# Kernel optimization log

Hardware: AMD Instinct MI355X
Metric: run time of the kernel (lower is better)

The kernel has to match this reference:

```python
import jax, jax.numpy as jnp
import numpy as np
from jax import lax

B, C, O, H, W = 4, 96, 96, 128, 128
K = 3      # kernel size everywhere
D = 2      # dilation of dconv
KK = K * K


def conv2d(x, w, b, pad, dil=1):
    # x: [B,C,H,W], w: [O,C,K,K]
    y = lax.conv_general_dilated(
        x, w, window_strides=(1, 1), padding=[(pad, pad), (pad, pad)],
        rhs_dilation=(dil, dil), dimension_numbers=('NCHW', 'OIHW', 'NCHW'))
    return y + b[None, :, None, None]


def bilinear_sample(img, py, px):
    # img: [B,C,H,W]; py,px: [B,KK,H,W] float sample coords (zero outside)
    y0 = jnp.floor(py)
    x0 = jnp.floor(px)
    wy = py - y0
    wx = px - x0
    flat = img.reshape(B, 1, C, H * W)  # broadcast over KK

    def gather(yi, xi):
        valid = (yi >= 0) & (yi < H) & (xi >= 0) & (xi < W)
        yc = jnp.clip(yi, 0, H - 1).astype(jnp.int32)
        xc = jnp.clip(xi, 0, W - 1).astype(jnp.int32)
        idx = (yc * W + xc).reshape(B, KK, 1, H * W)
        g = jnp.take_along_axis(flat, idx, axis=3)  # [B,KK,C,H*W]
        g = g.reshape(B, KK, C, H, W)
        return g * valid.reshape(B, KK, 1, H, W)

    v00 = gather(y0, x0)
    v01 = gather(y0, x0 + 1)
    v10 = gather(y0 + 1, x0)
    v11 = gather(y0 + 1, x0 + 1)
    wy = wy[:, :, None]
    wx = wx[:, :, None]
    return ((1 - wy) * ((1 - wx) * v00 + wx * v01)
            + wy * ((1 - wx) * v10 + wx * v11))


def setup_inputs() -> dict:
    key = jax.random.key(0)
    ks = jax.random.split(key, 7)
    x = jax.random.normal(ks[0], (B, C, H, W), jnp.float32)
    s = 1.0 / np.sqrt(C * K * K)  # torch default conv init bound
    u = lambda k, shape: jax.random.uniform(k, shape, jnp.float32, -s, s)
    return dict(
        x=x,
        dconv_w=u(ks[1], (O, C, K, K)), dconv_b=u(ks[2], (O,)),
        off_w=u(ks[3], (2 * KK, C, K, K)), off_b=u(ks[4], (2 * KK,)),
        def_w=u(ks[5], (O, C, K, K)), def_b=u(ks[6], (O,)),
    )


def reference(x, dconv_w, dconv_b, off_w, off_b, def_w, def_b):
    # dilated conv + relu + residual (self.conv is unused in the original forward)
    x1 = conv2d(x, dconv_w, dconv_b, pad=D, dil=D)
    x3 = x + jax.nn.relu(x1)

    # offset prediction: [B, 2*KK, H, W] -> (dy, dx) per kernel tap
    offset = conv2d(x3, off_w, off_b, pad=1)
    off = offset.reshape(B, KK, 2, H, W)
    dy, dx = off[:, :, 0], off[:, :, 1]

    # base sampling grid: output pixel + kernel tap - padding
    ki, kj = jnp.meshgrid(jnp.arange(K), jnp.arange(K), indexing='ij')
    ky = (ki.reshape(-1) - (K - 1) // 2).astype(jnp.float32)  # [KK]
    kx = (kj.reshape(-1) - (K - 1) // 2).astype(jnp.float32)
    ygrid = jnp.arange(H, dtype=jnp.float32)[:, None]
    xgrid = jnp.arange(W, dtype=jnp.float32)[None, :]
    py = ygrid[None, None] + ky[None, :, None, None] + dy  # [B,KK,H,W]
    px = xgrid[None, None] + kx[None, :, None, None] + dx

    sampled = bilinear_sample(x3, py, px)  # [B,KK,C,H,W]
    out = jnp.einsum('bkchw,ock->bohw', sampled, def_w.reshape(O, C, KK))
    return out + def_b[None, :, None, None]
```

## Files before the change

### kernel.cpp

```cpp
#include <hip/hip_runtime.h>
#include <hip/hip_bf16.h>

#define BD 4
#define CD 96
#define OD 96
#define HD 128
#define WD 128
#define HWD (HD*WD)

typedef __attribute__((ext_vector_type(8))) short bfrag;
typedef __attribute__((ext_vector_type(4))) float ffrag;

__device__ __forceinline__ short f2bs(float f) {
    __hip_bfloat16 h = __float2bfloat16(f);
    return *reinterpret_cast<short*>(&h);
}

__device__ __forceinline__ int swizzle256(int gid) {
    return ((gid & 7) << 5) | (gid >> 3);
}

__global__ __launch_bounds__(256) void k_transpose(const float* __restrict__ x,
                                                   short* __restrict__ xb16) {
    __shared__ short tile[64 * 104];
    int pix0 = blockIdx.x * 64;
    int b = pix0 / HWD; int hw0 = pix0 % HWD;
    int tid = threadIdx.x;

    for (int e = tid; e < 96*16; e += 256) {
        int c = e >> 4, g = e & 15;
        float4 v = *(const float4*)(x + ((size_t)(b*96 + c))*HWD + hw0 + 4*g);
        tile[(4*g+0)*104 + c] = f2bs(v.x);
        tile[(4*g+1)*104 + c] = f2bs(v.y);
        tile[(4*g+2)*104 + c] = f2bs(v.z);
        tile[(4*g+3)*104 + c] = f2bs(v.w);
    }
    __syncthreads();
    for (int e = tid; e < 64*12; e += 256) {
        int px = e / 12, c8 = e % 12;
        bfrag v = *(const bfrag*)(tile + px*104 + c8*8);
        *(bfrag*)(xb16 + ((size_t)(pix0 + px))*96 + c8*8) = v;
    }
}

__global__ void k_repack(const float* __restrict__ dconv_w,
                         const float* __restrict__ off_w,
                         const float* __restrict__ def_w,
                         short* __restrict__ wB1,
                         short* __restrict__ wB2,
                         short* __restrict__ wB) {
    int t = blockIdx.x * blockDim.x + threadIdx.x;
    if (t < 27648) {
        int j = t & 7; int l = (t >> 3) & 63; int tile = t >> 9;
        int s = tile >> 1, nt = tile & 1;
        int k = 32*s + (l >> 4)*8 + j;
        int o = 16*nt + (l & 15);
        int c = k % 96, tap = k / 96;
        wB2[t] = (o < 18) ? f2bs(off_w[(o*96 + c)*9 + tap]) : (short)0;
    }
    if (t < 82944) {
        int j = t & 7; int l = (t >> 3) & 63; int tile = t >> 9;
        int s = tile / 6, nt = tile % 6;
        int k = 32*s + (l >> 4)*8 + j;
        int o = 16*nt + (l & 15);
        int c = k % 96, tap = k / 96;
        wB1[t] = f2bs(dconv_w[(o*96 + c)*9 + tap]);
        wB[t]  = f2bs(def_w [(o*96 + c)*9 + tap]);
    }
}

#define SLICE_SHORTS 9216

__global__ __launch_bounds__(512, 2) void k_conv1(const float* __restrict__ x,
                                                  const short* __restrict__ xb16,
                                                  const short* __restrict__ wB,
                                                  const float* __restrict__ bias,
                                                  short* __restrict__ x3b) {
    __shared__ short wbuf[2][SLICE_SHORTS];

    int pix0 = swizzle256(blockIdx.x) * 256;
    int b = pix0 / HWD; int hw0 = pix0 % HWD;
    int h0 = hw0 / WD;
    int tid = threadIdx.x;
    int l = tid & 63, wv = tid >> 6;
    int q = l >> 4, mr = l & 15;
    const char* xbc = (const char*)(xb16 + ((size_t)b * HWD) * 96);
    const bfrag az = {0,0,0,0,0,0,0,0};

    int lpb[2], yb[2], wbx[2];
    #pragma unroll
    for (int mt = 0; mt < 2; mt++) {
        lpb[mt] = 32*wv + 16*mt;
        yb[mt]  = h0 + (lpb[mt] >> 7);
        wbx[mt] = (lpb[mt] & 127) + mr;
    }

    {
        bfrag s0, s1, s2;
        int c0 = tid, c1 = tid + 512, c2 = tid + 1024;
        s0 = *(const bfrag*)(wB + c0*8);
        s1 = *(const bfrag*)(wB + c1*8);
        if (c2 < 1152) s2 = *(const bfrag*)(wB + c2*8);
        *(bfrag*)&wbuf[0][c0*8] = s0;
        *(bfrag*)&wbuf[0][c1*8] = s1;
        if (c2 < 1152) *(bfrag*)&wbuf[0][c2*8] = s2;
    }
    __syncthreads();

    ffrag acc[2][6];
    #pragma unroll
    for (int mt = 0; mt < 2; mt++)
        #pragma unroll
        for (int nt = 0; nt < 6; nt++) acc[mt][nt] = ffrag{0.f,0.f,0.f,0.f};

    int cur = 0;
    #pragma unroll 1
    for (int tap = 0; tap < 9; tap++) {
        bfrag s0, s1, s2;
        if (tap < 8) {
            const short* src = wB + (size_t)(tap+1)*SLICE_SHORTS;
            int c2 = tid + 1024;
            s0 = *(const bfrag*)(src + tid*8);
            s1 = *(const bfrag*)(src + (tid+512)*8);
            if (c2 < 1152) s2 = *(const bfrag*)(src + c2*8);
        }

        int ty = (tap/3)*2 - 2, tx = (tap%3)*2 - 2;
        #pragma unroll
        for (int mt = 0; mt < 2; mt++) {
            int y = yb[mt] + ty;
            bool vy = (unsigned)y < HD;
            int yc = min(max(y, 0), HD-1);
            int xx = wbx[mt] + tx;
            int xxc = min(max(xx, 0), WD-1);
            bool v = vy && ((unsigned)xx < WD);
            unsigned aoff = (unsigned)(((yc*WD + xxc)*96 + q*8) * 2);
            #pragma unroll
            for (int sc = 0; sc < 3; sc++) {
                bfrag a = *(const bfrag*)(xbc + aoff + sc*64);
                if (!v) a = az;
                const short* wp = &wbuf[cur][(sc*6)*512 + l*8];
                #pragma unroll
                for (int nt = 0; nt < 6; nt++) {
                    bfrag bb = *(const bfrag*)(wp + nt*512);
                    acc[mt][nt] = __builtin_amdgcn_mfma_f32_16x16x32_bf16(a, bb, acc[mt][nt], 0, 0, 0);
                }
            }
        }

        if (tap < 8) {
            int c2 = tid + 1024;
            *(bfrag*)&wbuf[cur^1][tid*8]       = s0;
            *(bfrag*)&wbuf[cur^1][(tid+512)*8] = s1;
            if (c2 < 1152) *(bfrag*)&wbuf[cur^1][c2*8] = s2;
        }
        __syncthreads();
        cur ^= 1;
    }

    #pragma unroll
    for (int mt = 0; mt < 2; mt++) {
        int hwb = hw0 + lpb[mt] + q*4;
        #pragma unroll
        for (int nt = 0; nt < 6; nt++) {
            int o = 16*nt + mr;
            float bo = bias[o];
            float4 xr = *(const float4*)(x + ((size_t)(b*96 + o))*HWD + hwb);
            short* op = x3b + ((size_t)(b*HWD + hwb))*96 + o;
            op[0]   = f2bs(xr.x + fmaxf(acc[mt][nt][0] + bo, 0.f));
            op[96]  = f2bs(xr.y + fmaxf(acc[mt][nt][1] + bo, 0.f));
            op[192] = f2bs(xr.z + fmaxf(acc[mt][nt][2] + bo, 0.f));
            op[288] = f2bs(xr.w + fmaxf(acc[mt][nt][3] + bo, 0.f));
        }
    }
}

__global__ __launch_bounds__(512, 2) void k_deform(const short* __restrict__ x3b,
                                                   const short* __restrict__ wB2,
                                                   const float* __restrict__ off_b,
                                                   const short* __restrict__ wB,
                                                   const float* __restrict__ def_b,
                                                   float* __restrict__ out) {
    __shared__ short wbuf[2][SLICE_SHORTS];
    __shared__ float offsb[256][20];

    int pix0 = swizzle256(blockIdx.x) * 256;
    int b = pix0 / HWD; int hw0 = pix0 % HWD;
    int h0 = hw0 / WD;
    int tid = threadIdx.x;
    int l = tid & 63, wv = tid >> 6;
    int q = l >> 4, mr = l & 15;
    const char* xbc = (const char*)(x3b + ((size_t)b * HWD) * 96);
    const bfrag az = {0,0,0,0,0,0,0,0};

    int lpb[2], yb[2], wbx[2];
    #pragma unroll
    for (int mt = 0; mt < 2; mt++) {
        lpb[mt] = 32*wv + 16*mt;
        yb[mt]  = h0 + (lpb[mt] >> 7);
        wbx[mt] = (lpb[mt] & 127) + mr;
    }

    {
        bfrag s0, s1, s2;
        int c2 = tid + 1024;
        s0 = *(const bfrag*)(wB + tid*8);
        s1 = *(const bfrag*)(wB + (tid+512)*8);
        if (c2 < 1152) s2 = *(const bfrag*)(wB + c2*8);
        *(bfrag*)&wbuf[0][tid*8]       = s0;
        *(bfrag*)&wbuf[0][(tid+512)*8] = s1;
        if (c2 < 1152) *(bfrag*)&wbuf[0][c2*8] = s2;
    }
    __syncthreads();

    ffrag oa[2][2];
    #pragma unroll
    for (int mt = 0; mt < 2; mt++)
        #pragma unroll
        for (int nt = 0; nt < 2; nt++) oa[mt][nt] = ffrag{0.f,0.f,0.f,0.f};

    #pragma unroll 1
    for (int tap = 0; tap < 9; tap++) {
        int ty = tap/3 - 1, tx = tap%3 - 1;
        #pragma unroll
        for (int mt = 0; mt < 2; mt++) {
            int y = yb[mt] + ty;
            bool vy = (unsigned)y < HD;
            int yc = min(max(y, 0), HD-1);
            int xx = wbx[mt] + tx;
            int xxc = min(max(xx, 0), WD-1);
            bool v = vy && ((unsigned)xx < WD);
            unsigned aoff = (unsigned)(((yc*WD + xxc)*96 + q*8) * 2);
            #pragma unroll
            for (int sc = 0; sc < 3; sc++) {
                const short* wb = wB2 + ((size_t)((tap*3+sc)*2)*64 + l)*8;
                bfrag b0 = *(const bfrag*)(wb);
                bfrag b1 = *(const bfrag*)(wb + 512);
                bfrag a = *(const bfrag*)(xbc + aoff + sc*64);
                if (!v) a = az;
                oa[mt][0] = __builtin_amdgcn_mfma_f32_16x16x32_bf16(a, b0, oa[mt][0], 0, 0, 0);
                oa[mt][1] = __builtin_amdgcn_mfma_f32_16x16x32_bf16(a, b1, oa[mt][1], 0, 0, 0);
            }
        }
    }
    #pragma unroll
    for (int mt = 0; mt < 2; mt++) {
        int row = lpb[mt] + q*4;
        float bo0 = off_b[mr];
        #pragma unroll
        for (int r = 0; r < 4; r++) offsb[row + r][mr] = oa[mt][0][r] + bo0;
        if (mr < 2) {
            float bo1 = off_b[16 + mr];
            #pragma unroll
            for (int r = 0; r < 4; r++) offsb[row + r][16 + mr] = oa[mt][1][r] + bo1;
        }
    }

    ffrag acc[2][6];
    #pragma unroll
    for (int mt = 0; mt < 2; mt++)
        #pragma unroll
        for (int nt = 0; nt < 6; nt++) acc[mt][nt] = ffrag{0.f,0.f,0.f,0.f};

    int cur = 0;
    #pragma unroll 1
    for (int tap = 0; tap < 9; tap++) {
        bfrag s0, s1, s2;
        if (tap < 8) {
            const short* src = wB + (size_t)(tap+1)*SLICE_SHORTS;
            int c2 = tid + 1024;
            s0 = *(const bfrag*)(src + tid*8);
            s1 = *(const bfrag*)(src + (tid+512)*8);
            if (c2 < 1152) s2 = *(const bfrag*)(src + c2*8);
        }

        unsigned po[2][4];
        float fb[2][4];
        #pragma unroll
        for (int mt = 0; mt < 2; mt++) {
            int lp = lpb[mt] + mr;
            float dy = offsb[lp][2*tap];
            float dx = offsb[lp][2*tap + 1];
            float py  = (float)(yb[mt]  + tap/3 - 1) + dy;
            float pxf = (float)(wbx[mt] + tap%3 - 1) + dx;
            float y0f = floorf(py), x0f = floorf(pxf);
            float wy = py - y0f, wx = pxf - x0f;
            int y0 = (int)y0f, x0 = (int)x0f;
            int y1 = y0 + 1, x1 = x0 + 1;
            bool vy0 = (unsigned)y0 < HD, vy1 = (unsigned)y1 < HD;
            bool vx0 = (unsigned)x0 < WD, vx1 = (unsigned)x1 < WD;
            fb[mt][0] = (vy0 && vx0) ? (1.f-wy)*(1.f-wx) : 0.f;
            fb[mt][1] = (vy0 && vx1) ? (1.f-wy)*wx       : 0.f;
            fb[mt][2] = (vy1 && vx0) ? wy*(1.f-wx)       : 0.f;
            fb[mt][3] = (vy1 && vx1) ? wy*wx             : 0.f;
            int yc0 = min(max(y0,0),HD-1), yc1 = min(max(y1,0),HD-1);
            int xc0 = min(max(x0,0),WD-1), xc1 = min(max(x1,0),WD-1);
            po[mt][0] = (unsigned)(((yc0*WD + xc0)*96 + q*8)*2);
            po[mt][1] = (unsigned)(((yc0*WD + xc1)*96 + q*8)*2);
            po[mt][2] = (unsigned)(((yc1*WD + xc0)*96 + q*8)*2);
            po[mt][3] = (unsigned)(((yc1*WD + xc1)*96 + q*8)*2);
        }
        #pragma unroll
        for (int sc = 0; sc < 3; sc++) {
            const short* wp = &wbuf[cur][(sc*6)*512 + l*8];
            bfrag bbf[6];
            #pragma unroll
            for (int nt = 0; nt < 6; nt++) bbf[nt] = *(const bfrag*)(wp + nt*512);
            #pragma unroll
            for (int mt = 0; mt < 2; mt++) {
                bfrag c00 = *(const bfrag*)(xbc + po[mt][0] + sc*64);
                bfrag c01 = *(const bfrag*)(xbc + po[mt][1] + sc*64);
                bfrag c10 = *(const bfrag*)(xbc + po[mt][2] + sc*64);
                bfrag c11 = *(const bfrag*)(xbc + po[mt][3] + sc*64);
                const int* i00 = (const int*)&c00;
                const int* i01 = (const int*)&c01;
                const int* i10 = (const int*)&c10;
                const int* i11 = (const int*)&c11;
                float f00 = fb[mt][0], f01 = fb[mt][1];
                float f10 = fb[mt][2], f11 = fb[mt][3];
                int ap[4];
                #pragma unroll
                for (int d = 0; d < 4; d++) {
                    float a0 = __int_as_float(((unsigned)i00[d]) << 16);
                    float b0f = __int_as_float(((unsigned)i01[d]) << 16);
                    float c0f = __int_as_float(((unsigned)i10[d]) << 16);
                    float d0 = __int_as_float(((unsigned)i11[d]) << 16);
                    float a1 = __int_as_float(i00[d] & 0xffff0000);
                    float b1f = __int_as_float(i01[d] & 0xffff0000);
                    float c1f = __int_as_float(i10[d] & 0xffff0000);
                    float d1 = __int_as_float(i11[d] & 0xffff0000);
                    float rlo = f00*a0 + f01*b0f + f10*c0f + f11*d0;
                    float rhi = f00*a1 + f01*b1f + f10*c1f + f11*d1;
                    ap[d] = (int)((unsigned short)f2bs(rlo)) |
                            ((int)((unsigned short)f2bs(rhi)) << 16);
                }
                bfrag a = *(const bfrag*)ap;
                #pragma unroll
                for (int nt = 0; nt < 6; nt++)
                    acc[mt][nt] = __builtin_amdgcn_mfma_f32_16x16x32_bf16(a, bbf[nt], acc[mt][nt], 0, 0, 0);
            }
        }

        if (tap < 8) {
            int c2 = tid + 1024;
            *(bfrag*)&wbuf[cur^1][tid*8]       = s0;
            *(bfrag*)&wbuf[cur^1][(tid+512)*8] = s1;
            if (c2 < 1152) *(bfrag*)&wbuf[cur^1][c2*8] = s2;
        }
        __syncthreads();
        cur ^= 1;
    }

    #pragma unroll
    for (int mt = 0; mt < 2; mt++) {
        int hwb = hw0 + lpb[mt] + q*4;
        #pragma unroll
        for (int nt = 0; nt < 6; nt++) {
            int o = 16*nt + mr;
            float bo = def_b[o];
            float4 v;
            v.x = acc[mt][nt][0] + bo; v.y = acc[mt][nt][1] + bo;
            v.z = acc[mt][nt][2] + bo; v.w = acc[mt][nt][3] + bo;
            *(float4*)(out + ((size_t)(b*96 + o))*HWD + hwb) = v;
        }
    }
}

extern "C" void kernel_launch(void* const* d_in, const int* in_sizes, int n_in,
                              void* d_out, int out_size, void* d_ws, size_t ws_size,
                              hipStream_t stream) {
    const float* x       = (const float*)d_in[0];
    const float* dconv_w = (const float*)d_in[1];
    const float* dconv_b = (const float*)d_in[2];
    const float* off_w   = (const float*)d_in[3];
    const float* off_b   = (const float*)d_in[4];
    const float* def_w   = (const float*)d_in[5];
    const float* def_b   = (const float*)d_in[6];
    float* out = (float*)d_out;

    char* ws = (char*)d_ws;
    short* xb16 = (short*)(ws);
    short* x3b  = (short*)(ws + 12582912);
    short* wB1  = (short*)(ws + 25165824);
    short* wB2  = (short*)(ws + 25331712);
    short* wB   = (short*)(ws + 25387008);

    k_repack<<<324, 256, 0, stream>>>(dconv_w, off_w, def_w, wB1, wB2, wB);
    k_transpose<<<(BD*HWD)/64, 256, 0, stream>>>(x, xb16);
    k_conv1<<<(BD*HWD)/256, 512, 0, stream>>>(x, xb16, wB1, dconv_b, x3b);
    k_deform<<<(BD*HWD)/256, 512, 0, stream>>>(x3b, wB2, off_b, wB, def_b, out);
}
```

Baseline: 162.3 us.

## Stage x3 epilogue via LDS, LDS-buffer offset weights, prefetch next-tap gathers

The dconv epilogue now stages bf16 x3 results in an LDS tile and writes full 16-byte channel vectors per pixel, replacing scattered 2-byte global stores. In the deform kernel, offset-conv weights are double-buffered in shared memory instead of being read from global inside the MFMA loop. The first channel chunk of the next tap's bilinear gathers is prefetched during the current tap to hide gather latency. The cost is more shared memory, extra barriers in the offset loop, and higher register pressure from the prefetched fragments, which may reduce occupancy under launch bounds of 512 threads and 2 blocks.

```diff
diff --git a/kernel.cpp b/kernel.cpp
--- a/kernel.cpp
+++ b/kernel.cpp
@@ -14,6 +14,31 @@
 __device__ __forceinline__ short f2bs(float f) {
     __hip_bfloat16 h = __float2bfloat16(f);
     return *reinterpret_cast<short*>(&h);
+}
+
+__device__ __forceinline__ bfrag interp4(bfrag c00, bfrag c01, bfrag c10, bfrag c11,
+                                         float f00, float f01, float f10, float f11) {
+    const int* i00 = (const int*)&c00;
+    const int* i01 = (const int*)&c01;
+    const int* i10 = (const int*)&c10;
+    const int* i11 = (const int*)&c11;
+    int ap[4];
+    #pragma unroll
+    for (int d = 0; d < 4; d++) {
+        float a0 = __int_as_float(((unsigned)i00[d]) << 16);
+        float b0 = __int_as_float(((unsigned)i01[d]) << 16);
+        float c0 = __int_as_float(((unsigned)i10[d]) << 16);
+        float d0 = __int_as_float(((unsigned)i11[d]) << 16);
+        float a1 = __int_as_float(i00[d] & 0xffff0000);
+        float b1 = __int_as_float(i01[d] & 0xffff0000);
+        float c1 = __int_as_float(i10[d] & 0xffff0000);
+        float d1 = __int_as_float(i11[d] & 0xffff0000);
+        float rlo = f00*a0 + f01*b0 + f10*c0 + f11*d0;
+        float rhi = f00*a1 + f01*b1 + f10*c1 + f11*d1;
+        ap[d] = (int)((unsigned short)f2bs(rlo)) |
+                ((int)((unsigned short)f2bs(rhi)) << 16);
+    }
+    return *(const bfrag*)ap;
 }
 
 __device__ __forceinline__ int swizzle256(int gid) {
@@ -97,12 +122,12 @@
 
     {
         bfrag s0, s1, s2;
-        int c0 = tid, c1 = tid + 512, c2 = tid + 1024;
-        s0 = *(const bfrag*)(wB + c0*8);
-        s1 = *(const bfrag*)(wB + c1*8);
+        int c2 = tid + 1024;
+        s0 = *(const bfrag*)(wB + tid*8);
+        s1 = *(const bfrag*)(wB + (tid+512)*8);
         if (c2 < 1152) s2 = *(const bfrag*)(wB + c2*8);
-        *(bfrag*)&wbuf[0][c0*8] = s0;
-        *(bfrag*)&wbuf[0][c1*8] = s1;
+        *(bfrag*)&wbuf[0][tid*8]       = s0;
+        *(bfrag*)&wbuf[0][(tid+512)*8] = s1;
         if (c2 < 1152) *(bfrag*)&wbuf[0][c2*8] = s2;
     }
     __syncthreads();
@@ -158,20 +183,33 @@
         cur ^= 1;
     }
 
-    #pragma unroll
-    for (int mt = 0; mt < 2; mt++) {
-        int hwb = hw0 + lpb[mt] + q*4;
-        #pragma unroll
-        for (int nt = 0; nt < 6; nt++) {
-            int o = 16*nt + mr;
-            float bo = bias[o];
-            float4 xr = *(const float4*)(x + ((size_t)(b*96 + o))*HWD + hwb);
-            short* op = x3b + ((size_t)(b*HWD + hwb))*96 + o;
-            op[0]   = f2bs(xr.x + fmaxf(acc[mt][nt][0] + bo, 0.f));
-            op[96]  = f2bs(xr.y + fmaxf(acc[mt][nt][1] + bo, 0.f));
-            op[192] = f2bs(xr.z + fmaxf(acc[mt][nt][2] + bo, 0.f));
-            op[288] = f2bs(xr.w + fmaxf(acc[mt][nt][3] + bo, 0.f));
-        }
+    short (*etile)[104] = (short(*)[104])&wbuf[0][0];
+    #pragma unroll 1
+    for (int ph = 0; ph < 2; ph++) {
+        #pragma unroll
+        for (int mt = 0; mt < 2; mt++) {
+            if ((lpb[mt] >> 7) == ph) {
+                int lrow = (lpb[mt] & 127) + q*4;
+                int hwb = hw0 + 128*ph + lrow;
+                #pragma unroll
+                for (int nt = 0; nt < 6; nt++) {
+                    int o = 16*nt + mr;
+                    float bo = bias[o];
+                    float4 xr = *(const float4*)(x + ((size_t)(b*96 + o))*HWD + hwb);
+                    etile[lrow+0][o] = f2bs(xr.x + fmaxf(acc[mt][nt][0] + bo, 0.f));
+                    etile[lrow+1][o] = f2bs(xr.y + fmaxf(acc[mt][nt][1] + bo, 0.f));
+                    etile[lrow+2][o] = f2bs(xr.z + fmaxf(acc[mt][nt][2] + bo, 0.f));
+                    etile[lrow+3][o] = f2bs(xr.w + fmaxf(acc[mt][nt][3] + bo, 0.f));
+                }
+            }
+        }
+        __syncthreads();
+        for (int e = tid; e < 128*12; e += 512) {
+            int px = e / 12, c8 = e % 12;
+            bfrag v = *(const bfrag*)&etile[px][c8*8];
+            *(bfrag*)(x3b + ((size_t)(b*HWD + hw0 + 128*ph + px))*96 + c8*8) = v;
+        }
+        __syncthreads();
     }
 }
 
@@ -181,8 +219,10 @@
                                                    const short* __restrict__ wB,
                                                    const float* __restrict__ def_b,
                                                    float* __restrict__ out) {
-    __shared__ short wbuf[2][SLICE_SHORTS];
-    __shared__ float offsb[256][20];
+    __shared__ __align__(16) char smem[36864 + 20480];
+    short (*wbuf)[SLICE_SHORTS] = (short(*)[SLICE_SHORTS])smem;
+    short* cb = (short*)(smem + 36864);
+    float (*offsb)[20] = (float(*)[20])(smem + 36864);
 
     int pix0 = swizzle256(blockIdx.x) * 256;
     int b = pix0 / HWD; int hw0 = pix0 % HWD;
@@ -210,6 +250,10 @@
         *(bfrag*)&wbuf[0][tid*8]       = s0;
         *(bfrag*)&wbuf[0][(tid+512)*8] = s1;
         if (c2 < 1152) *(bfrag*)&wbuf[0][c2*8] = s2;
+        if (tid < 384) {
+            bfrag sc2 = *(const bfrag*)(wB2 + tid*8);
+            *(bfrag*)&cb[tid*8] = sc2;
+        }
     }
     __syncthreads();
 
@@ -219,8 +263,13 @@
         #pragma unroll
         for (int nt = 0; nt < 2; nt++) oa[mt][nt] = ffrag{0.f,0.f,0.f,0.f};
 
+    int c2cur = 0;
     #pragma unroll 1
     for (int tap = 0; tap < 9; tap++) {
+        bfrag sn;
+        bool act = (tid < 384) && (tap < 8);
+        if (act) sn = *(const bfrag*)(wB2 + (size_t)(tap+1)*3072 + tid*8);
+
         int ty = tap/3 - 1, tx = tap%3 - 1;
         #pragma unroll
         for (int mt = 0; mt < 2; mt++) {
@@ -233,7 +282,7 @@
             unsigned aoff = (unsigned)(((yc*WD + xxc)*96 + q*8) * 2);
             #pragma unroll
             for (int sc = 0; sc < 3; sc++) {
-                const short* wb = wB2 + ((size_t)((tap*3+sc)*2)*64 + l)*8;
+                const short* wb = cb + c2cur*3072 + (sc*2)*512 + l*8;
                 bfrag b0 = *(const bfrag*)(wb);
                 bfrag b1 = *(const bfrag*)(wb + 512);
                 bfrag a = *(const bfrag*)(xbc + aoff + sc*64);
@@ -242,7 +291,12 @@
                 oa[mt][1] = __builtin_amdgcn_mfma_f32_16x16x32_bf16(a, b1, oa[mt][1], 0, 0, 0);
             }
         }
-    }
+
+        if (act) *(bfrag*)&cb[(c2cur^1)*3072 + tid*8] = sn;
+        __syncthreads();
+        c2cur ^= 1;
+    }
+
     #pragma unroll
     for (int mt = 0; mt < 2; mt++) {
         int row = lpb[mt] + q*4;
@@ -262,20 +316,7 @@
         #pragma unroll
         for (int nt = 0; nt < 6; nt++) acc[mt][nt] = ffrag{0.f,0.f,0.f,0.f};
 
-    int cur = 0;
-    #pragma unroll 1
-    for (int tap = 0; tap < 9; tap++) {
-        bfrag s0, s1, s2;
-        if (tap < 8) {
-            const short* src = wB + (size_t)(tap+1)*SLICE_SHORTS;
-            int c2 = tid + 1024;
-            s0 = *(const bfrag*)(src + tid*8);
-            s1 = *(const bfrag*)(src + (tid+512)*8);
-            if (c2 < 1152) s2 = *(const bfrag*)(src + c2*8);
-        }
-
-        unsigned po[2][4];
-        float fb[2][4];
+    auto prep = [&](int tap, unsigned (&po)[2][4], float (&fbv)[2][4]) {
         #pragma unroll
         for (int mt = 0; mt < 2; mt++) {
             int lp = lpb[mt] + mr;
@@ -289,10 +330,10 @@
             int y1 = y0 + 1, x1 = x0 + 1;
             bool vy0 = (unsigned)y0 < HD, vy1 = (unsigned)y1 < HD;
             bool vx0 = (unsigned)x0 < WD, vx1 = (unsigned)x1 < WD;
-            fb[mt][0] = (vy0 && vx0) ? (1.f-wy)*(1.f-wx) : 0.f;
-            fb[mt][1] = (vy0 && vx1) ? (1.f-wy)*wx       : 0.f;
-            fb[mt][2] = (vy1 && vx0) ? wy*(1.f-wx)       : 0.f;
-            fb[mt][3] = (vy1 && vx1) ? wy*wx             : 0.f;
+            fbv[mt][0] = (vy0 && vx0) ? (1.f-wy)*(1.f-wx) : 0.f;
+            fbv[mt][1] = (vy0 && vx1) ? (1.f-wy)*wx       : 0.f;
+            fbv[mt][2] = (vy1 && vx0) ? wy*(1.f-wx)       : 0.f;
+            fbv[mt][3] = (vy1 && vx1) ? wy*wx             : 0.f;
             int yc0 = min(max(y0,0),HD-1), yc1 = min(max(y1,0),HD-1);
             int xc0 = min(max(x0,0),WD-1), xc1 = min(max(x1,0),WD-1);
             po[mt][0] = (unsigned)(((yc0*WD + xc0)*96 + q*8)*2);
@@ -300,8 +341,53 @@
             po[mt][2] = (unsigned)(((yc1*WD + xc0)*96 + q*8)*2);
             po[mt][3] = (unsigned)(((yc1*WD + xc1)*96 + q*8)*2);
         }
-        #pragma unroll
-        for (int sc = 0; sc < 3; sc++) {
+    };
+
+    unsigned po[2][4]; float fbv[2][4];
+    prep(0, po, fbv);
+    bfrag cpre[8];
+    #pragma unroll
+    for (int mt = 0; mt < 2; mt++)
+        #pragma unroll
+        for (int k = 0; k < 4; k++)
+            cpre[mt*4+k] = *(const bfrag*)(xbc + po[mt][k]);
+
+    int cur = 0;
+    #pragma unroll 1
+    for (int tap = 0; tap < 9; tap++) {
+        bfrag s0, s1, s2;
+        if (tap < 8) {
+            const short* src = wB + (size_t)(tap+1)*SLICE_SHORTS;
+            int c2 = tid + 1024;
+            s0 = *(const bfrag*)(src + tid*8);
+            s1 = *(const bfrag*)(src + (tid+512)*8);
+            if (c2 < 1152) s2 = *(const bfrag*)(src + c2*8);
+        }
+        unsigned pon[2][4]; float fbn[2][4]; bfrag cnx[8];
+        if (tap < 8) {
+            prep(tap+1, pon, fbn);
+            #pragma unroll
+            for (int mt = 0; mt < 2; mt++)
+                #pragma unroll
+                for (int k = 0; k < 4; k++)
+                    cnx[mt*4+k] = *(const bfrag*)(xbc + pon[mt][k]);
+        }
+        {
+            const short* wp = &wbuf[cur][0*512 + l*8];
+            bfrag bbf[6];
+            #pragma unroll
+            for (int nt = 0; nt < 6; nt++) bbf[nt] = *(const bfrag*)(wp + nt*512);
+            #pragma unroll
+            for (int mt = 0; mt < 2; mt++) {
+                bfrag a = interp4(cpre[mt*4+0], cpre[mt*4+1], cpre[mt*4+2], cpre[mt*4+3],
+                                  fbv[mt][0], fbv[mt][1], fbv[mt][2], fbv[mt][3]);
+                #pragma unroll
+                for (int nt = 0; nt < 6; nt++)
+                    acc[mt][nt] = __builtin_amdgcn_mfma_f32_16x16x32_bf16(a, bbf[nt], acc[mt][nt], 0, 0, 0);
+            }
+        }
+        #pragma unroll
+        for (int sc = 1; sc < 3; sc++) {
             const short* wp = &wbuf[cur][(sc*6)*512 + l*8];
             bfrag bbf[6];
             #pragma unroll
@@ -312,40 +398,27 @@
                 bfrag c01 = *(const bfrag*)(xbc + po[mt][1] + sc*64);
                 bfrag c10 = *(const bfrag*)(xbc + po[mt][2] + sc*64);
                 bfrag c11 = *(const bfrag*)(xbc + po[mt][3] + sc*64);
-                const int* i00 = (const int*)&c00;
-                const int* i01 = (const int*)&c01;
-                const int* i10 = (const int*)&c10;
-                const int* i11 = (const int*)&c11;
-                float f00 = fb[mt][0], f01 = fb[mt][1];
-                float f10 = fb[mt][2], f11 = fb[mt][3];
-                int ap[4];
-                #pragma unroll
-                for (int d = 0; d < 4; d++) {
-                    float a0 = __int_as_float(((unsigned)i00[d]) << 16);
-                    float b0f = __int_as_float(((unsigned)i01[d]) << 16);
-                    float c0f = __int_as_float(((unsigned)i10[d]) << 16);
-                    float d0 = __int_as_float(((unsigned)i11[d]) << 16);
-                    float a1 = __int_as_float(i00[d] & 0xffff0000);
-                    float b1f = __int_as_float(i01[d] & 0xffff0000);
-                    float c1f = __int_as_float(i10[d] & 0xffff0000);
-                    float d1 = __int_as_float(i11[d] & 0xffff0000);
-                    float rlo = f00*a0 + f01*b0f + f10*c0f + f11*d0;
-                    float rhi = f00*a1 + f01*b1f + f10*c1f + f11*d1;
-                    ap[d] = (int)((unsigned short)f2bs(rlo)) |
-                            ((int)((unsigned short)f2bs(rhi)) << 16);
-                }
-                bfrag a = *(const bfrag*)ap;
+                bfrag a = interp4(c00, c01, c10, c11,
+                                  fbv[mt][0], fbv[mt][1], fbv[mt][2], fbv[mt][3]);
                 #pragma unroll
                 for (int nt = 0; nt < 6; nt++)
                     acc[mt][nt] = __builtin_amdgcn_mfma_f32_16x16x32_bf16(a, bbf[nt], acc[mt][nt], 0, 0, 0);
             }
         }
-
         if (tap < 8) {
             int c2 = tid + 1024;
             *(bfrag*)&wbuf[cur^1][tid*8]       = s0;
             *(bfrag*)&wbuf[cur^1][(tid+512)*8] = s1;
             if (c2 < 1152) *(bfrag*)&wbuf[cur^1][c2*8] = s2;
+            #pragma unroll
+            for (int mt = 0; mt < 2; mt++)
+                #pragma unroll
+                for (int k = 0; k < 4; k++) {
+                    po[mt][k] = pon[mt][k];
+                    fbv[mt][k] = fbn[mt][k];
+                }
+            #pragma unroll
+            for (int k = 0; k < 8; k++) cpre[k] = cnx[k];
         }
         __syncthreads();
         cur ^= 1;
```

Result: slower. 168.1 us (+3.6%).

## Halve per-block pixel tile, stage offset weights and x3 stores through LDS

Applied to the files above, without the earlier changes.

Both conv kernels now process one image row (128 pixels) per 512-thread block instead of 256 pixels, doubling the grid and halving per-wave accumulators, with a matching swizzle. The conv1 epilogue writes into an LDS tile and then stores x3b with coalesced 16-byte vectors instead of scattered 2-byte stores. The offset-conv weights in k_deform are now double-buffered in LDS rather than read from global memory in the inner loop. The added cost is that each block reloads the full weight slices for only half the pixels, doubling weight traffic, and there are extra barriers.

```diff
diff --git a/kernel.cpp b/kernel.cpp
--- a/kernel.cpp
+++ b/kernel.cpp
@@ -16,8 +16,33 @@
     return *reinterpret_cast<short*>(&h);
 }
 
-__device__ __forceinline__ int swizzle256(int gid) {
-    return ((gid & 7) << 5) | (gid >> 3);
+__device__ __forceinline__ bfrag interp4(bfrag c00, bfrag c01, bfrag c10, bfrag c11,
+                                         float f00, float f01, float f10, float f11) {
+    const int* i00 = (const int*)&c00;
+    const int* i01 = (const int*)&c01;
+    const int* i10 = (const int*)&c10;
+    const int* i11 = (const int*)&c11;
+    int ap[4];
+    #pragma unroll
+    for (int d = 0; d < 4; d++) {
+        float a0 = __int_as_float(((unsigned)i00[d]) << 16);
+        float b0 = __int_as_float(((unsigned)i01[d]) << 16);
+        float c0 = __int_as_float(((unsigned)i10[d]) << 16);
+        float d0 = __int_as_float(((unsigned)i11[d]) << 16);
+        float a1 = __int_as_float(i00[d] & 0xffff0000);
+        float b1 = __int_as_float(i01[d] & 0xffff0000);
+        float c1 = __int_as_float(i10[d] & 0xffff0000);
+        float d1 = __int_as_float(i11[d] & 0xffff0000);
+        float rlo = f00*a0 + f01*b0 + f10*c0 + f11*d0;
+        float rhi = f00*a1 + f01*b1 + f10*c1 + f11*d1;
+        ap[d] = (int)((unsigned short)f2bs(rlo)) |
+                ((int)((unsigned short)f2bs(rhi)) << 16);
+    }
+    return *(const bfrag*)ap;
+}
+
+__device__ __forceinline__ int swizzle512(int gid) {
+    return ((gid & 7) << 6) | (gid >> 3);
 }
 
 __global__ __launch_bounds__(256) void k_transpose(const float* __restrict__ x,
@@ -78,40 +103,31 @@
                                                   short* __restrict__ x3b) {
     __shared__ short wbuf[2][SLICE_SHORTS];
 
-    int pix0 = swizzle256(blockIdx.x) * 256;
+    int pix0 = swizzle512(blockIdx.x) * 128;
     int b = pix0 / HWD; int hw0 = pix0 % HWD;
-    int h0 = hw0 / WD;
+    int h = hw0 / WD;
     int tid = threadIdx.x;
     int l = tid & 63, wv = tid >> 6;
     int q = l >> 4, mr = l & 15;
+    int px0w = 16*wv;
     const char* xbc = (const char*)(xb16 + ((size_t)b * HWD) * 96);
     const bfrag az = {0,0,0,0,0,0,0,0};
 
-    int lpb[2], yb[2], wbx[2];
-    #pragma unroll
-    for (int mt = 0; mt < 2; mt++) {
-        lpb[mt] = 32*wv + 16*mt;
-        yb[mt]  = h0 + (lpb[mt] >> 7);
-        wbx[mt] = (lpb[mt] & 127) + mr;
-    }
-
     {
         bfrag s0, s1, s2;
-        int c0 = tid, c1 = tid + 512, c2 = tid + 1024;
-        s0 = *(const bfrag*)(wB + c0*8);
-        s1 = *(const bfrag*)(wB + c1*8);
+        int c2 = tid + 1024;
+        s0 = *(const bfrag*)(wB + tid*8);
+        s1 = *(const bfrag*)(wB + (tid+512)*8);
         if (c2 < 1152) s2 = *(const bfrag*)(wB + c2*8);
-        *(bfrag*)&wbuf[0][c0*8] = s0;
-        *(bfrag*)&wbuf[0][c1*8] = s1;
+        *(bfrag*)&wbuf[0][tid*8]       = s0;
+        *(bfrag*)&wbuf[0][(tid+512)*8] = s1;
         if (c2 < 1152) *(bfrag*)&wbuf[0][c2*8] = s2;
     }
     __syncthreads();
 
-    ffrag acc[2][6];
+    ffrag acc[6];
     #pragma unroll
-    for (int mt = 0; mt < 2; mt++)
-        #pragma unroll
-        for (int nt = 0; nt < 6; nt++) acc[mt][nt] = ffrag{0.f,0.f,0.f,0.f};
+    for (int nt = 0; nt < 6; nt++) acc[nt] = ffrag{0.f,0.f,0.f,0.f};
 
     int cur = 0;
     #pragma unroll 1
@@ -125,26 +141,21 @@
             if (c2 < 1152) s2 = *(const bfrag*)(src + c2*8);
         }
 
-        int ty = (tap/3)*2 - 2, tx = (tap%3)*2 - 2;
-        #pragma unroll
-        for (int mt = 0; mt < 2; mt++) {
-            int y = yb[mt] + ty;
-            bool vy = (unsigned)y < HD;
-            int yc = min(max(y, 0), HD-1);
-            int xx = wbx[mt] + tx;
-            int xxc = min(max(xx, 0), WD-1);
-            bool v = vy && ((unsigned)xx < WD);
-            unsigned aoff = (unsigned)(((yc*WD + xxc)*96 + q*8) * 2);
+        int y = h + (tap/3)*2 - 2;
+        int yc = min(max(y, 0), HD-1);
+        int xx = px0w + mr + (tap%3)*2 - 2;
+        int xxc = min(max(xx, 0), WD-1);
+        bool v = ((unsigned)y < HD) && ((unsigned)xx < WD);
+        unsigned aoff = (unsigned)(((yc*WD + xxc)*96 + q*8) * 2);
+        #pragma unroll
+        for (int sc = 0; sc < 3; sc++) {
+            bfrag a = *(const bfrag*)(xbc + aoff + sc*64);
+            if (!v) a = az;
+            const short* wp = &wbuf[cur][(sc*6)*512 + l*8];
             #pragma unroll
-            for (int sc = 0; sc < 3; sc++) {
-                bfrag a = *(const bfrag*)(xbc + aoff + sc*64);
-                if (!v) a = az;
-                const short* wp = &wbuf[cur][(sc*6)*512 + l*8];
-                #pragma unroll
-                for (int nt = 0; nt < 6; nt++) {
-                    bfrag bb = *(const bfrag*)(wp + nt*512);
-                    acc[mt][nt] = __builtin_amdgcn_mfma_f32_16x16x32_bf16(a, bb, acc[mt][nt], 0, 0, 0);
-                }
+            for (int nt = 0; nt < 6; nt++) {
+                bfrag bb = *(const bfrag*)(wp + nt*512);
+                acc[nt] = __builtin_amdgcn_mfma_f32_16x16x32_bf16(a, bb, acc[nt], 0, 0, 0);
             }
         }
 
@@ -158,20 +169,26 @@
         cur ^= 1;
     }
 
-    #pragma unroll
-    for (int mt = 0; mt < 2; mt++) {
-        int hwb = hw0 + lpb[mt] + q*4;
+    short (*etile)[104] = (short(*)[104])&wbuf[0][0];
+    {
+        int lrow = px0w + q*4;
+        int hwb = hw0 + lrow;
         #pragma unroll
         for (int nt = 0; nt < 6; nt++) {
             int o = 16*nt + mr;
             float bo = bias[o];
             float4 xr = *(const float4*)(x + ((size_t)(b*96 + o))*HWD + hwb);
-            short* op = x3b + ((size_t)(b*HWD + hwb))*96 + o;
-            op[0]   = f2bs(xr.x + fmaxf(acc[mt][nt][0] + bo, 0.f));
-            op[96]  = f2bs(xr.y + fmaxf(acc[mt][nt][1] + bo, 0.f));
-            op[192] = f2bs(xr.z + fmaxf(acc[mt][nt][2] + bo, 0.f));
-            op[288] = f2bs(xr.w + fmaxf(acc[mt][nt][3] + bo, 0.f));
-        }
+            etile[lrow+0][o] = f2bs(xr.x + fmaxf(acc[nt][0] + bo, 0.f));
+            etile[lrow+1][o] = f2bs(xr.y + fmaxf(acc[nt][1] + bo, 0.f));
+            etile[lrow+2][o] = f2bs(xr.z + fmaxf(acc[nt][2] + bo, 0.f));
+            etile[lrow+3][o] = f2bs(xr.w + fmaxf(acc[nt][3] + bo, 0.f));
+        }
+    }
+    __syncthreads();
+    for (int e = tid; e < 128*12; e += 512) {
+        int px = e / 12, c8 = e % 12;
+        bfrag v = *(const bfrag*)&etile[px][c8*8];
+        *(bfrag*)(x3b + ((size_t)(b*HWD + hw0 + px))*96 + c8*8) = v;
     }
 }
 
@@ -181,25 +198,20 @@
                                                    const short* __restrict__ wB,
                                                    const float* __restrict__ def_b,
                                                    float* __restrict__ out) {
-    __shared__ short wbuf[2][SLICE_SHORTS];
-    __shared__ float offsb[256][20];
-
-    int pix0 = swizzle256(blockIdx.x) * 256;
+    __shared__ __align__(16) char smem[36864 + 12288];
+    short (*wbuf)[SLICE_SHORTS] = (short(*)[SLICE_SHORTS])smem;
+    short* cb = (short*)(smem + 36864);
+    float (*offsb)[20] = (float(*)[20])(smem + 36864);
+
+    int pix0 = swizzle512(blockIdx.x) * 128;
     int b = pix0 / HWD; int hw0 = pix0 % HWD;
-    int h0 = hw0 / WD;
+    int h = hw0 / WD;
     int tid = threadIdx.x;
     int l = tid & 63, wv = tid >> 6;
     int q = l >> 4, mr = l & 15;
+    int px0w = 16*wv;
     const char* xbc = (const char*)(x3b + ((size_t)b * HWD) * 96);
     const bfrag az = {0,0,0,0,0,0,0,0};
-
-    int lpb[2], yb[2], wbx[2];
-    #pragma unroll
-    for (int mt = 0; mt < 2; mt++) {
-        lpb[mt] = 32*wv + 16*mt;
-        yb[mt]  = h0 + (lpb[mt] >> 7);
-        wbx[mt] = (lpb[mt] & 127) + mr;
-    }
 
     {
         bfrag s0, s1, s2;
@@ -210,57 +222,60 @@
         *(bfrag*)&wbuf[0][tid*8]       = s0;
         *(bfrag*)&wbuf[0][(tid+512)*8] = s1;
         if (c2 < 1152) *(bfrag*)&wbuf[0][c2*8] = s2;
+        if (tid < 384) {
+            bfrag sc2 = *(const bfrag*)(wB2 + tid*8);
+            *(bfrag*)&cb[tid*8] = sc2;
+        }
     }
     __syncthreads();
 
-    ffrag oa[2][2];
-    #pragma unroll
-    for (int mt = 0; mt < 2; mt++)
-        #pragma unroll
-        for (int nt = 0; nt < 2; nt++) oa[mt][nt] = ffrag{0.f,0.f,0.f,0.f};
-
+    ffrag oa0 = ffrag{0.f,0.f,0.f,0.f};
+    ffrag oa1 = ffrag{0.f,0.f,0.f,0.f};
+
+    int c2cur = 0;
     #pragma unroll 1
     for (int tap = 0; tap < 9; tap++) {
-        int ty = tap/3 - 1, tx = tap%3 - 1;
-        #pragma unroll
-        for (int mt = 0; mt < 2; mt++) {
-            int y = yb[mt] + ty;
-            bool vy = (unsigned)y < HD;
-            int yc = min(max(y, 0), HD-1);
-            int xx = wbx[mt] + tx;
-            int xxc = min(max(xx, 0), WD-1);
-            bool v = vy && ((unsigned)xx < WD);
-            unsigned aoff = (unsigned)(((yc*WD + xxc)*96 + q*8) * 2);
-            #pragma unroll
-            for (int sc = 0; sc < 3; sc++) {
-                const short* wb = wB2 + ((size_t)((tap*3+sc)*2)*64 + l)*8;
-                bfrag b0 = *(const bfrag*)(wb);
-                bfrag b1 = *(const bfrag*)(wb + 512);
-                bfrag a = *(const bfrag*)(xbc + aoff + sc*64);
-                if (!v) a = az;
-                oa[mt][0] = __builtin_amdgcn_mfma_f32_16x16x32_bf16(a, b0, oa[mt][0], 0, 0, 0);
-                oa[mt][1] = __builtin_amdgcn_mfma_f32_16x16x32_bf16(a, b1, oa[mt][1], 0, 0, 0);
-            }
-        }
-    }
-    #pragma unroll
-    for (int mt = 0; mt < 2; mt++) {
-        int row = lpb[mt] + q*4;
+        bfrag sn;
+        bool act = (tid < 384) && (tap < 8);
+        if (act) sn = *(const bfrag*)(wB2 + (size_t)(tap+1)*3072 + tid*8);
+
+        int y = h + tap/3 - 1;
+        int yc = min(max(y, 0), HD-1);
+        int xx = px0w + mr + tap%3 - 1;
+        int xxc = min(max(xx, 0), WD-1);
+        bool v = ((unsigned)y < HD) && ((unsigned)xx < WD);
+        unsigned aoff = (unsigned)(((yc*WD + xxc)*96 + q*8) * 2);
+        #pragma unroll
+        for (int sc = 0; sc < 3; sc++) {
+            const short* wb = cb + c2cur*3072 + (sc*2)*512 + l*8;
+            bfrag b0 = *(const bfrag*)(wb);
+            bfrag b1 = *(const bfrag*)(wb + 512);
+            bfrag a = *(const bfrag*)(xbc + aoff + sc*64);
+            if (!v) a = az;
+            oa0 = __builtin_amdgcn_mfma_f32_16x16x32_bf16(a, b0, oa0, 0, 0, 0);
+            oa1 = __builtin_amdgcn_mfma_f32_16x16x32_bf16(a, b1, oa1, 0, 0, 0);
+        }
+
+        if (act) *(bfrag*)&cb[(c2cur^1)*3072 + tid*8] = sn;
+        __syncthreads();
+        c2cur ^= 1;
+    }
+
+    {
+        int row = px0w + q*4;
         float bo0 = off_b[mr];
         #pragma unroll
-        for (int r = 0; r < 4; r++) offsb[row + r][mr] = oa[mt][0][r] + bo0;
+        for (int r = 0; r < 4; r++) offsb[row + r][mr] = oa0[r] + bo0;
         if (mr < 2) {
             float bo1 = off_b[16 + mr];
             #pragma unroll
-            for (int r = 0; r < 4; r++) offsb[row + r][16 + mr] = oa[mt][1][r] + bo1;
-        }
-    }
-
-    ffrag acc[2][6];
+            for (int r = 0; r < 4; r++) offsb[row + r][16 + mr] = oa1[r] + bo1;
+        }
+    }
+
+    ffrag acc[6];
     #pragma unroll
-    for (int mt = 0; mt < 2; mt++)
-        #pragma unroll
-        for (int nt = 0; nt < 6; nt++) acc[mt][nt] = ffrag{0.f,0.f,0.f,0.f};
+    for (int nt = 0; nt < 6; nt++) acc[nt] = ffrag{0.f,0.f,0.f,0.f};
 
     int cur = 0;
     #pragma unroll 1
@@ -274,31 +289,30 @@
             if (c2 < 1152) s2 = *(const bfrag*)(src + c2*8);
         }
 
-        unsigned po[2][4];
-        float fb[2][4];
-        #pragma unroll
-        for (int mt = 0; mt < 2; mt++) {
-            int lp = lpb[mt] + mr;
+        unsigned po[4];
+        float fbv[4];
+        {
+            int lp = px0w + mr;
             float dy = offsb[lp][2*tap];
             float dx = offsb[lp][2*tap + 1];
-            float py  = (float)(yb[mt]  + tap/3 - 1) + dy;
-            float pxf = (float)(wbx[mt] + tap%3 - 1) + dx;
+            float py  = (float)(h  + tap/3 - 1) + dy;
+            float pxf = (float)(lp + tap%3 - 1) + dx;
             float y0f = floorf(py), x0f = floorf(pxf);
             float wy = py - y0f, wx = pxf - x0f;
             int y0 = (int)y0f, x0 = (int)x0f;
             int y1 = y0 + 1, x1 = x0 + 1;
             bool vy0 = (unsigned)y0 < HD, vy1 = (unsigned)y1 < HD;
             bool vx0 = (unsigned)x0 < WD, vx1 = (unsigned)x1 < WD;
-            fb[mt][0] = (vy0 && vx0) ? (1.f-wy)*(1.f-wx) : 0.f;
-            fb[mt][1] = (vy0 && vx1) ? (1.f-wy)*wx       : 0.f;
-            fb[mt][2] = (vy1 && vx0) ? wy*(1.f-wx)       : 0.f;
-            fb[mt][3] = (vy1 && vx1) ? wy*wx             : 0.f;
+            fbv[0] = (vy0 && vx0) ? (1.f-wy)*(1.f-wx) : 0.f;
+            fbv[1] = (vy0 && vx1) ? (1.f-wy)*wx       : 0.f;
+            fbv[2] = (vy1 && vx0) ? wy*(1.f-wx)       : 0.f;
+            fbv[3] = (vy1 && vx1) ? wy*wx             : 0.f;
             int yc0 = min(max(y0,0),HD-1), yc1 = min(max(y1,0),HD-1);
             int xc0 = min(max(x0,0),WD-1), xc1 = min(max(x1,0),WD-1);
-            po[mt][0] = (unsigned)(((yc0*WD + xc0)*96 + q*8)*2);
-            po[mt][1] = (unsigned)(((yc0*WD + xc1)*96 + q*8)*2);
-            po[mt][2] = (unsigned)(((yc1*WD + xc0)*96 + q*8)*2);
-            po[mt][3] = (unsigned)(((yc1*WD + xc1)*96 + q*8)*2);
+            po[0] = (unsigned)(((yc0*WD + xc0)*96 + q*8)*2);
+            po[1] = (unsigned)(((yc0*WD + xc1)*96 + q*8)*2);
+            po[2] = (unsigned)(((yc1*WD + xc0)*96 + q*8)*2);
+            po[3] = (unsigned)(((yc1*WD + xc1)*96 + q*8)*2);
         }
         #pragma unroll
         for (int sc = 0; sc < 3; sc++) {
@@ -306,39 +320,14 @@
             bfrag bbf[6];
             #pragma unroll
             for (int nt = 0; nt < 6; nt++) bbf[nt] = *(const bfrag*)(wp + nt*512);
+            bfrag c00 = *(const bfrag*)(xbc + po[0] + sc*64);
+            bfrag c01 = *(const bfrag*)(xbc + po[1] + sc*64);
+            bfrag c10 = *(const bfrag*)(xbc + po[2] + sc*64);
+            bfrag c11 = *(const bfrag*)(xbc + po[3] + sc*64);
+            bfrag a = interp4(c00, c01, c10, c11, fbv[0], fbv[1], fbv[2], fbv[3]);
             #pragma unroll
-            for (int mt = 0; mt < 2; mt++) {
-                bfrag c00 = *(const bfrag*)(xbc + po[mt][0] + sc*64);
-                bfrag c01 = *(const bfrag*)(xbc + po[mt][1] + sc*64);
-                bfrag c10 = *(const bfrag*)(xbc + po[mt][2] + sc*64);
-                bfrag c11 = *(const bfrag*)(xbc + po[mt][3] + sc*64);
-                const int* i00 = (const int*)&c00;
-                const int* i01 = (const int*)&c01;
-                const int* i10 = (const int*)&c10;
-                const int* i11 = (const int*)&c11;
-                float f00 = fb[mt][0], f01 = fb[mt][1];
-                float f10 = fb[mt][2], f11 = fb[mt][3];
-                int ap[4];
-                #pragma unroll
-                for (int d = 0; d < 4; d++) {
-                    float a0 = __int_as_float(((unsigned)i00[d]) << 16);
-                    float b0f = __int_as_float(((unsigned)i01[d]) << 16);
-                    float c0f = __int_as_float(((unsigned)i10[d]) << 16);
-                    float d0 = __int_as_float(((unsigned)i11[d]) << 16);
-                    float a1 = __int_as_float(i00[d] & 0xffff0000);
-                    float b1f = __int_as_float(i01[d] & 0xffff0000);
-                    float c1f = __int_as_float(i10[d] & 0xffff0000);
-                    float d1 = __int_as_float(i11[d] & 0xffff0000);
-                    float rlo = f00*a0 + f01*b0f + f10*c0f + f11*d0;
-                    float rhi = f00*a1 + f01*b1f + f10*c1f + f11*d1;
-                    ap[d] = (int)((unsigned short)f2bs(rlo)) |
-                            ((int)((unsigned short)f2bs(rhi)) << 16);
-                }
-                bfrag a = *(const bfrag*)ap;
-                #pragma unroll
-                for (int nt = 0; nt < 6; nt++)
-                    acc[mt][nt] = __builtin_amdgcn_mfma_f32_16x16x32_bf16(a, bbf[nt], acc[mt][nt], 0, 0, 0);
-            }
+            for (int nt = 0; nt < 6; nt++)
+                acc[nt] = __builtin_amdgcn_mfma_f32_16x16x32_bf16(a, bbf[nt], acc[nt], 0, 0, 0);
         }
 
         if (tap < 8) {
@@ -351,18 +340,15 @@
         cur ^= 1;
     }
 
+    int hwb = hw0 + px0w + q*4;
     #pragma unroll
-    for (int mt = 0; mt < 2; mt++) {
-        int hwb = hw0 + lpb[mt] + q*4;
-        #pragma unroll
-        for (int nt = 0; nt < 6; nt++) {
-            int o = 16*nt + mr;
-            float bo = def_b[o];
-            float4 v;
-            v.x = acc[mt][nt][0] + bo; v.y = acc[mt][nt][1] + bo;
-            v.z = acc[mt][nt][2] + bo; v.w = acc[mt][nt][3] + bo;
-            *(float4*)(out + ((size_t)(b*96 + o))*HWD + hwb) = v;
-        }
+    for (int nt = 0; nt < 6; nt++) {
+        int o = 16*nt + mr;
+        float bo = def_b[o];
+        float4 v;
+        v.x = acc[nt][0] + bo; v.y = acc[nt][1] + bo;
+        v.z = acc[nt][2] + bo; v.w = acc[nt][3] + bo;
+        *(float4*)(out + ((size_t)(b*96 + o))*HWD + hwb) = v;
     }
 }
 
@@ -387,6 +373,6 @@
 
     k_repack<<<324, 256, 0, stream>>>(dconv_w, off_w, def_w, wB1, wB2, wB);
     k_transpose<<<(BD*HWD)/64, 256, 0, stream>>>(x, xb16);
-    k_conv1<<<(BD*HWD)/256, 512, 0, stream>>>(x, xb16, wB1, dconv_b, x3b);
-    k_deform<<<(BD*HWD)/256, 512, 0, stream>>>(x3b, wB2, off_b, wB, def_b, out);
-}
+    k_conv1<<<(BD*HWD)/128, 512, 0, stream>>>(x, xb16, wB1, dconv_b, x3b);
+    k_deform<<<(BD*HWD)/128, 512, 0, stream>>>(x3b, wB2, off_b, wB, def_b, out);
+}
```

After: 160.7 us. No clear change (-1.0%).
